# Kernel tuning notes

Hardware: AMD Instinct MI355X
Metric: run time of the kernel (lower is better)

The kernel has to match this reference:

```python
import jax, jax.numpy as jnp
import numpy as np

D_MODEL = 1024
NUM_HEADS = 16
D_K = D_MODEL // NUM_HEADS


def setup_inputs() -> dict:
    key = jax.random.key(0)
    ks = jax.random.split(key, 9)
    s = 1.0 / np.sqrt(D_MODEL)
    inp = {
        "x": jax.random.normal(ks[0], (4, 2048, D_MODEL), dtype=jnp.float32),
        "W_q": jax.random.uniform(ks[1], (D_MODEL, D_MODEL), jnp.float32, -s, s),
        "b_q": jax.random.uniform(ks[2], (D_MODEL,), jnp.float32, -s, s),
        "W_k": jax.random.uniform(ks[3], (D_MODEL, D_MODEL), jnp.float32, -s, s),
        "b_k": jax.random.uniform(ks[4], (D_MODEL,), jnp.float32, -s, s),
        "W_v": jax.random.uniform(ks[5], (D_MODEL, D_MODEL), jnp.float32, -s, s),
        "b_v": jax.random.uniform(ks[6], (D_MODEL,), jnp.float32, -s, s),
        "W_o": jax.random.uniform(ks[7], (D_MODEL, D_MODEL), jnp.float32, -s, s),
        "b_o": jax.random.uniform(ks[8], (D_MODEL,), jnp.float32, -s, s),
    }
    return inp


def reference(x, W_q, b_q, W_k, b_k, W_v, b_v, W_o, b_o):
    B, S, _ = x.shape
    # Linear layers (torch convention: y = x @ W.T + b), split into heads -> [B, H, S, d_k]
    def proj(W, b):
        y = jnp.einsum("bsd,ed->bse", x, W) + b
        return y.reshape(B, S, NUM_HEADS, D_K).transpose(0, 2, 1, 3)

    Q = proj(W_q, b_q)
    K = proj(W_k, b_k)
    V = proj(W_v, b_v)

    scale = 1.0 / jnp.sqrt(jnp.asarray(D_K, dtype=x.dtype))
    scores = jnp.einsum("bhqd,bhkd->bhqk", Q, K) * scale  # [B, H, S, S]
    attn = jax.nn.softmax(scores, axis=-1)
    out = jnp.einsum("bhqk,bhkd->bhqd", attn, V)  # [B, H, S, d_k]
    out = out.transpose(0, 2, 1, 3).reshape(B, S, D_MODEL)
    return jnp.einsum("bsd,ed->bse", out, W_o) + b_o
```

## Files before the change

### kernel.cpp

```cpp
#include <hip/hip_runtime.h>
#include <hip/hip_bf16.h>
#include <math.h>


constexpr int D = 1024;
constexpr int H = 16;
constexpr int DK = 64;
constexpr int PSTR = 72;

typedef unsigned short u16;
typedef __attribute__((ext_vector_type(8))) short v8s;
typedef __attribute__((ext_vector_type(4))) float v4f;
typedef const __attribute__((address_space(1))) void gvoid;
typedef __attribute__((address_space(3))) void lvoid;
typedef __attribute__((address_space(3))) u16 ls_u16;
typedef __attribute__((address_space(3))) v8s lv8s;

__device__ __forceinline__ u16 rne_bf16(float f) {
  unsigned u = __float_as_uint(f);
  u += 0x7FFFu + ((u >> 16) & 1u);
  return (u16)(u >> 16);
}

__device__ __forceinline__ unsigned pk_bf16(float a, float b) {
  __hip_bfloat162 t = __float22bfloat162_rn(float2{a, b});
  return *reinterpret_cast<unsigned*>(&t);
}

__device__ __forceinline__ void cfence() { asm volatile("" ::: "memory"); }

__device__ __forceinline__ void split_body(const float* __restrict__ in,
                                           u16* __restrict__ hi, u16* __restrict__ lo,
                                           int i)
{
  const float4 v = ((const float4*)in)[i];
  const float f[4] = {v.x, v.y, v.z, v.w};
  ushort4 h, l;
  u16 hh[4], ll[4];
#pragma unroll
  for (int j = 0; j < 4; ++j) {
    const unsigned u = __float_as_uint(f[j]);
    hh[j] = (u16)(u >> 16);
    const float hf = __uint_as_float(u & 0xFFFF0000u);
    ll[j] = rne_bf16(f[j] - hf);
  }
  h.x = hh[0]; h.y = hh[1]; h.z = hh[2]; h.w = hh[3];
  l.x = ll[0]; l.y = ll[1]; l.z = ll[2]; l.w = ll[3];
  ((ushort4*)hi)[i] = h;
  ((ushort4*)lo)[i] = l;
}

__global__ __launch_bounds__(256) void split_all_kernel(
    const float* __restrict__ x,
    const float* __restrict__ w0, const float* __restrict__ w1,
    const float* __restrict__ w2, const float* __restrict__ w3,
    u16* __restrict__ xs_hi, u16* __restrict__ xs_lo,
    u16* __restrict__ qkv_hi, u16* __restrict__ qkv_lo,
    u16* __restrict__ o_hi, u16* __restrict__ o_lo, int n4x)
{
  constexpr int N4W = (int)(D * (size_t)D / 4);
  const int i = blockIdx.x * 256 + threadIdx.x;
  if (i < n4x) {
    split_body(x, xs_hi, xs_lo, i);
    return;
  }
  const int t = i - n4x;
  const int y = t / N4W;
  const int j = t - y * N4W;
  if (y >= 4) return;
  const float* src = (y == 0) ? w0 : (y == 1) ? w1 : (y == 2) ? w2 : w3;
  const size_t off = (size_t)y * (size_t)(D * (size_t)D);
  u16* hi = (y < 3) ? qkv_hi + off : o_hi;
  u16* lo = (y < 3) ? qkv_lo + off : o_lo;
  split_body(src, hi, lo, j);
}

template<int R>
__device__ __forceinline__ void stage_arr(const u16* __restrict__ src, ls_u16* dst,
                                          int tid, int row0, int k0)
{
  const int cg = (tid & 3) ^ ((tid >> 3) & 3);
#pragma unroll
  for (int j = 0; j < R / 128; ++j) {
    const int row = j * 128 + (tid >> 2);
    __builtin_amdgcn_global_load_lds(
        (gvoid*)(src + (size_t)(row0 + row) * D + k0 + cg * 8),
        (lvoid*)(dst + j * 4096 + tid * 8), 16, 0, 0);
  }
}

template<int BM, int BN, int EPI>
__global__ __launch_bounds__(512, 2) void gemm_pipe_kernel(
    const u16* __restrict__ Ahi, const u16* __restrict__ Alo,
    const u16* __restrict__ Whi, const u16* __restrict__ Wlo,
    const float* __restrict__ b0v, const float* __restrict__ b1v, const float* __restrict__ b2v,
    u16* __restrict__ Qb, u16* __restrict__ Kb, u16* __restrict__ Vtb,
    float* __restrict__ C, int S_)
{
  constexpr int TA = BM * 32;
  constexpr int TB = BN * 32;
  constexpr int BUFSZ = 2 * TA + 2 * TB;
  __shared__ u16 lds[3][BUFSZ];

  const int tid = threadIdx.x;
  const int lane = tid & 63, w = tid >> 6;
  const int wm = (w >> 1) * 64, wn = (w & 1) * 64;
  const int fr = lane & 15, fq = lane >> 4;
  const int csw = (fq ^ ((fr >> 1) & 3)) * 8;

  const int gx = gridDim.x;
  const int gyd = gridDim.y;
  const int nwg = gx * gyd;
  int id = blockIdx.y * gx + blockIdx.x;
  id = (id & 7) * (nwg >> 3) + (id >> 3);
  constexpr int GM = 4;
  const int per_grp = GM * gyd;
  const int grp = id / per_grp;
  const int ing = id - grp * per_grp;
  const int m0 = (grp * GM + (ing & (GM - 1))) * BM;
  const int n0 = (ing / GM) * BN;

  v4f acc[4][4];
#pragma unroll
  for (int mi = 0; mi < 4; ++mi)
#pragma unroll
    for (int ni = 0; ni < 4; ++ni) acc[mi][ni] = (v4f){0.f, 0.f, 0.f, 0.f};

  ls_u16* pb0 = (ls_u16*)&lds[0][0];
  ls_u16* pb1 = (ls_u16*)&lds[1][0];
  ls_u16* pb2 = (ls_u16*)&lds[2][0];

  int aoff[4], boff[4];
#pragma unroll
  for (int i = 0; i < 4; ++i) {
    aoff[i] = (wm + i * 16 + fr) * 32 + csw;
    boff[i] = 2 * TA + (wn + i * 16 + fr) * 32 + csw;
  }

#pragma unroll
  for (int p = 0; p < 2; ++p) {
    ls_u16* pb = (p == 0) ? pb0 : pb1;
    stage_arr<BM>(Ahi, pb, tid, m0, p * 32);
    stage_arr<BM>(Alo, pb + TA, tid, m0, p * 32);
    stage_arr<BN>(Whi, pb + 2 * TA, tid, n0, p * 32);
    stage_arr<BN>(Wlo, pb + 2 * TA + TB, tid, n0, p * 32);
  }

#pragma unroll 2
  for (int k = 0; k < 32; ++k) {
    const int ks = (k + 2 < 32) ? (k + 2) * 32 : 31 * 32;

    asm volatile("s_waitcnt vmcnt(6)" ::: "memory");
    __builtin_amdgcn_s_barrier();
    cfence();

    v8s ah[4], bh[4], tf[4];
#pragma unroll
    for (int i = 0; i < 4; ++i) ah[i] = *(const lv8s*)(pb0 + aoff[i]);
#pragma unroll
    for (int i = 0; i < 4; ++i) bh[i] = *(const lv8s*)(pb0 + boff[i]);
    stage_arr<BM>(Ahi, pb2, tid, m0, ks);
    __builtin_amdgcn_s_setprio(1);
#pragma unroll
    for (int mi = 0; mi < 4; ++mi)
#pragma unroll
      for (int ni = 0; ni < 4; ++ni)
        acc[mi][ni] = __builtin_amdgcn_mfma_f32_16x16x32_bf16(ah[mi], bh[ni], acc[mi][ni], 0, 0, 0);
    __builtin_amdgcn_s_setprio(0);
    cfence();
    __builtin_amdgcn_s_barrier();
    cfence();

#pragma unroll
    for (int i = 0; i < 4; ++i) tf[i] = *(const lv8s*)(pb0 + TA + aoff[i]);
    stage_arr<BM>(Alo, pb2 + TA, tid, m0, ks);
    __builtin_amdgcn_s_setprio(1);
#pragma unroll
    for (int mi = 0; mi < 4; ++mi)
#pragma unroll
      for (int ni = 0; ni < 4; ++ni)
        acc[mi][ni] = __builtin_amdgcn_mfma_f32_16x16x32_bf16(tf[mi], bh[ni], acc[mi][ni], 0, 0, 0);
    __builtin_amdgcn_s_setprio(0);
    cfence();
    __builtin_amdgcn_s_barrier();
    cfence();

#pragma unroll
    for (int i = 0; i < 4; ++i) tf[i] = *(const lv8s*)(pb0 + boff[i] + TB);
    stage_arr<BN>(Whi, pb2 + 2 * TA, tid, n0, ks);
    stage_arr<BN>(Wlo, pb2 + 2 * TA + TB, tid, n0, ks);
    __builtin_amdgcn_s_setprio(1);
#pragma unroll
    for (int mi = 0; mi < 4; ++mi)
#pragma unroll
      for (int ni = 0; ni < 4; ++ni)
        acc[mi][ni] = __builtin_amdgcn_mfma_f32_16x16x32_bf16(ah[mi], tf[ni], acc[mi][ni], 0, 0, 0);
    __builtin_amdgcn_s_setprio(0);
    cfence();

    ls_u16* t = pb0; pb0 = pb1; pb1 = pb2; pb2 = t;
  }

  const int lane4 = fq * 4;
  if constexpr (EPI == 0) {
    const int wsel = n0 >> 10;
    const float* bias = (wsel == 0) ? b0v : (wsel == 1) ? b1v : b2v;
    u16* Cb = (wsel == 0) ? Qb : (wsel == 1) ? Kb : Vtb;
    const int bb = m0 / S_;
    const int s0 = m0 - bb * S_;
#pragma unroll
    for (int mi = 0; mi < 4; ++mi) {
#pragma unroll
      for (int ni = 0; ni < 4; ++ni) {
        const int n = n0 + wn + ni * 16 + fr;
        const int nl = n & (D - 1);
        const float bvv = bias[nl];
        const int h = nl >> 6, dk = nl & 63;
#pragma unroll
        for (int r = 0; r < 4; ++r) {
          const int s = s0 + wm + mi * 16 + lane4 + r;
          const float val = acc[mi][ni][r] + bvv;
          if (wsel < 2)
            Cb[((size_t)(bb * H + h) * S_ + s) * DK + dk] = rne_bf16(val);
          else
            Cb[((size_t)(bb * H + h) * DK + dk) * S_ + s] = rne_bf16(val);
        }
      }
    }
  } else {
#pragma unroll
    for (int mi = 0; mi < 4; ++mi)
#pragma unroll
      for (int ni = 0; ni < 4; ++ni) {
        const int n = n0 + wn + ni * 16 + fr;
        const float bvv = b0v[n];
#pragma unroll
        for (int r = 0; r < 4; ++r) {
          const int m = m0 + wm + mi * 16 + lane4 + r;
          C[(size_t)m * D + n] = acc[mi][ni][r] + bvv;
        }
      }
  }
}

__global__ __launch_bounds__(512, 4) void attn_mfma_kernel(
    const u16* __restrict__ Qb, const u16* __restrict__ Kb, const u16* __restrict__ Vtb,
    u16* __restrict__ Ohi, u16* __restrict__ Olo, int S_)
{
  __shared__ u16 Ks[2][64 * 64];
  __shared__ u16 Vt[2][64 * 64];
  __shared__ u16 Pl[8][32 * PSTR];

  const int tid = threadIdx.x;
  const int lane = tid & 63, w = tid >> 6;
  const int fr = lane & 15, fq = lane >> 4;

  const int gqx = gridDim.x;
  const int nwg = gqx * gridDim.y * gridDim.z;
  int id = (blockIdx.z * gridDim.y + blockIdx.y) * gqx + blockIdx.x;
  id = (id & 7) * (nwg >> 3) + (id >> 3);
  const int qx = id % gqx;
  const int rest = id / gqx;
  const int h = rest % H;
  const int b = rest / H;

  const int q0 = qx * 256;
  const int wq = w * 32;
  const size_t base = (size_t)(b * H + h) * S_ * DK;

  const int srow = tid >> 3;
  const int scb = (tid & 7) ^ (srow & 7);

  auto stage_kv = [&](int j0, int bufi) {
    __builtin_amdgcn_global_load_lds((gvoid*)(Kb + base + (size_t)(j0 + srow) * DK + scb * 8),
                                     (lvoid*)(&Ks[bufi][0] + tid * 8), 16, 0, 0);
    __builtin_amdgcn_global_load_lds((gvoid*)(Vtb + base + (size_t)srow * S_ + j0 + scb * 8),
                                     (lvoid*)(&Vt[bufi][0] + tid * 8), 16, 0, 0);
  };

  stage_kv(0, 0);

  v8s qa[2][2];
#pragma unroll
  for (int ni = 0; ni < 2; ++ni)
#pragma unroll
    for (int ks = 0; ks < 2; ++ks)
      qa[ni][ks] = *(const v8s*)(Qb + base + (size_t)(q0 + wq + ni * 16 + fr) * DK + ks * 32 + fq * 8);

  v4f o[4][2];
  float lsum[2] = {0.f, 0.f};
#pragma unroll
  for (int mi = 0; mi < 4; ++mi)
#pragma unroll
    for (int ni = 0; ni < 2; ++ni) o[mi][ni] = (v4f){0.f, 0.f, 0.f, 0.f};

  asm volatile("s_waitcnt vmcnt(0)" ::: "memory");
  __builtin_amdgcn_s_barrier();
  cfence();

  const int NT = S_ >> 6;
  for (int jt = 0; jt < NT; ++jt) {
    const int cur = jt & 1;
    if (jt + 1 < NT) stage_kv((jt + 1) * 64, cur ^ 1);

    const u16* Kc = &Ks[cur][0];
    const u16* Vc = &Vt[cur][0];

    v4f s[4][2];
#pragma unroll
    for (int mi = 0; mi < 4; ++mi)
#pragma unroll
      for (int ni = 0; ni < 2; ++ni) s[mi][ni] = (v4f){0.f, 0.f, 0.f, 0.f};
#pragma unroll
    for (int ks = 0; ks < 2; ++ks) {
      v8s kb[4];
#pragma unroll
      for (int mi = 0; mi < 4; ++mi) {
        const int row = mi * 16 + fr;
        kb[mi] = *(const v8s*)&Kc[row * 64 + (((ks * 4 + fq) ^ (row & 7)) * 8)];
      }
#pragma unroll
      for (int mi = 0; mi < 4; ++mi)
#pragma unroll
        for (int ni = 0; ni < 2; ++ni)
          s[mi][ni] = __builtin_amdgcn_mfma_f32_16x16x32_bf16(kb[mi], qa[ni][ks], s[mi][ni], 0, 0, 0);
    }

#pragma unroll
    for (int mi = 0; mi < 4; ++mi)
#pragma unroll
      for (int ni = 0; ni < 2; ++ni) {
        float p[4];
#pragma unroll
        for (int r = 0; r < 4; ++r) p[r] = __expf(s[mi][ni][r] * 0.125f);
        lsum[ni] += (p[0] + p[1]) + (p[2] + p[3]);
        uint2 pk;
        pk.x = pk_bf16(p[0], p[1]);
        pk.y = pk_bf16(p[2], p[3]);
        *(uint2*)&Pl[w][(ni * 16 + fr) * PSTR + mi * 16 + fq * 4] = pk;
      }

#pragma unroll
    for (int ks = 0; ks < 2; ++ks) {
      v8s vb[4], pa[2];
#pragma unroll
      for (int mi = 0; mi < 4; ++mi) {
        const int row = mi * 16 + fr;
        vb[mi] = *(const v8s*)&Vc[row * 64 + (((ks * 4 + fq) ^ (row & 7)) * 8)];
      }
#pragma unroll
      for (int ni = 0; ni < 2; ++ni)
        pa[ni] = *(const v8s*)&Pl[w][(ni * 16 + fr) * PSTR + ks * 32 + fq * 8];
#pragma unroll
      for (int mi = 0; mi < 4; ++mi)
#pragma unroll
        for (int ni = 0; ni < 2; ++ni)
          o[mi][ni] = __builtin_amdgcn_mfma_f32_16x16x32_bf16(vb[mi], pa[ni], o[mi][ni], 0, 0, 0);
    }

    asm volatile("s_waitcnt vmcnt(0)" ::: "memory");
    cfence();
    __builtin_amdgcn_s_barrier();
    cfence();
  }

  float linv[2];
#pragma unroll
  for (int ni = 0; ni < 2; ++ni) {
    float l = lsum[ni];
    l += __shfl_xor(l, 16);
    l += __shfl_xor(l, 32);
    linv[ni] = 1.f / l;
  }

#pragma unroll
  for (int ni = 0; ni < 2; ++ni) {
    const int q = q0 + wq + ni * 16 + fr;
    const size_t rowbase = (size_t)(b * S_ + q) * D + h * DK;
#pragma unroll
    for (int mi = 0; mi < 4; ++mi) {
      const int d0 = mi * 16 + fq * 4;
      float v[4];
      unsigned u[4];
      float res[4];
#pragma unroll
      for (int r = 0; r < 4; ++r) {
        v[r] = o[mi][ni][r] * linv[ni];
        u[r] = __float_as_uint(v[r]);
        res[r] = v[r] - __uint_as_float(u[r] & 0xFFFF0000u);
      }
      uint2 hi, lo;
      hi.x = (u[1] & 0xFFFF0000u) | (u[0] >> 16);
      hi.y = (u[3] & 0xFFFF0000u) | (u[2] >> 16);
      lo.x = pk_bf16(res[0], res[1]);
      lo.y = pk_bf16(res[2], res[3]);
      *(uint2*)(Ohi + rowbase + d0) = hi;
      *(uint2*)(Olo + rowbase + d0) = lo;
    }
  }
}

extern "C" void kernel_launch(void* const* d_in, const int* in_sizes, int n_in,
                              void* d_out, int out_size, void* d_ws, size_t ws_size,
                              hipStream_t stream) {
  const float* x  = (const float*)d_in[0];
  const float* Wq = (const float*)d_in[1];
  const float* bq = (const float*)d_in[2];
  const float* Wk = (const float*)d_in[3];
  const float* bk = (const float*)d_in[4];
  const float* Wv = (const float*)d_in[5];
  const float* bv = (const float*)d_in[6];
  const float* Wo = (const float*)d_in[7];
  const float* bo = (const float*)d_in[8];

  const int M = in_sizes[0] / D;
  const int B = 4;
  const int S_ = M / B;
  const size_t MD = (size_t)M * D;
  const size_t DD = (size_t)D * D;

  u16* Qb    = (u16*)d_ws;
  u16* Kb    = Qb + MD;
  u16* Vtb   = Kb + MD;
  u16* xs_hi = Vtb + MD;
  u16* xs_lo = xs_hi + MD;
  u16* Ohi   = xs_lo + MD;
  u16* Olo   = Ohi + MD;
  u16* wo_hi = Olo + MD;
  u16* wo_lo = wo_hi + DD;

  u16* wqkv_hi = (u16*)d_out;
  u16* wqkv_lo = wqkv_hi + 3 * DD;

  const int n4x = (int)(MD / 4);
  const int n4w = (int)(DD / 4);
  const int nsb = (n4x + 4 * n4w + 255) / 256;
  split_all_kernel<<<nsb, 256, 0, stream>>>(x, Wq, Wk, Wv, Wo,
                                            xs_hi, xs_lo, wqkv_hi, wqkv_lo,
                                            wo_hi, wo_lo, n4x);

  dim3 gq(M / 256, 3 * D / 128);
  gemm_pipe_kernel<256, 128, 0><<<gq, 512, 0, stream>>>(
      xs_hi, xs_lo, wqkv_hi, wqkv_lo, bq, bk, bv, Qb, Kb, Vtb, nullptr, S_);

  dim3 ga(S_ / 256, H, B);
  attn_mfma_kernel<<<ga, 512, 0, stream>>>(Qb, Kb, Vtb, Ohi, Olo, S_);

  dim3 go(M / 256, D / 128);
  gemm_pipe_kernel<256, 128, 1><<<go, 512, 0, stream>>>(
      Ohi, Olo, wo_hi, wo_lo, bo, nullptr, nullptr, nullptr, nullptr, nullptr,
      (float*)d_out, S_);
}
```

Measured before the change: 394.1 us.

## Enlarge GEMM tiles to 256x256 and switch to double-buffered LDS pipeline

The projection GEMMs now use 256x256 output tiles with each wave computing 128x64, doubling per-wave accumulators to raise arithmetic intensity and cut global re-reads of the split bf16 operands. The LDS pipeline drops from triple to double buffering, prefetching only one k-step ahead and synchronising with a full vmcnt(0) wait plus barrier each iteration. This halves the grid size (fewer workgroups, e.g. 128 for the output projection) and raises register and LDS pressure (128KB LDS), so occupancy and latency hiding may suffer.

```diff
diff --git a/kernel.cpp b/kernel.cpp
--- a/kernel.cpp
+++ b/kernel.cpp
@@ -89,7 +89,7 @@
   }
 }
 
-template<int BM, int BN, int EPI>
+template<int EPI>
 __global__ __launch_bounds__(512, 2) void gemm_pipe_kernel(
     const u16* __restrict__ Ahi, const u16* __restrict__ Alo,
     const u16* __restrict__ Whi, const u16* __restrict__ Wlo,
@@ -97,14 +97,15 @@
     u16* __restrict__ Qb, u16* __restrict__ Kb, u16* __restrict__ Vtb,
     float* __restrict__ C, int S_)
 {
+  constexpr int BM = 256, BN = 256;
   constexpr int TA = BM * 32;
   constexpr int TB = BN * 32;
   constexpr int BUFSZ = 2 * TA + 2 * TB;
-  __shared__ u16 lds[3][BUFSZ];
+  __shared__ u16 lds[2][BUFSZ];
 
   const int tid = threadIdx.x;
   const int lane = tid & 63, w = tid >> 6;
-  const int wm = (w >> 1) * 64, wn = (w & 1) * 64;
+  const int wm = (w >> 2) * 128, wn = (w & 3) * 64;
   const int fr = lane & 15, fq = lane >> 4;
   const int csw = (fq ^ ((fr >> 1) & 3)) * 8;
 
@@ -120,49 +121,43 @@
   const int m0 = (grp * GM + (ing & (GM - 1))) * BM;
   const int n0 = (ing / GM) * BN;
 
-  v4f acc[4][4];
-#pragma unroll
-  for (int mi = 0; mi < 4; ++mi)
+  v4f acc[8][4];
+#pragma unroll
+  for (int mi = 0; mi < 8; ++mi)
 #pragma unroll
     for (int ni = 0; ni < 4; ++ni) acc[mi][ni] = (v4f){0.f, 0.f, 0.f, 0.f};
 
   ls_u16* pb0 = (ls_u16*)&lds[0][0];
   ls_u16* pb1 = (ls_u16*)&lds[1][0];
-  ls_u16* pb2 = (ls_u16*)&lds[2][0];
-
-  int aoff[4], boff[4];
-#pragma unroll
-  for (int i = 0; i < 4; ++i) {
-    aoff[i] = (wm + i * 16 + fr) * 32 + csw;
-    boff[i] = 2 * TA + (wn + i * 16 + fr) * 32 + csw;
-  }
-
-#pragma unroll
-  for (int p = 0; p < 2; ++p) {
-    ls_u16* pb = (p == 0) ? pb0 : pb1;
-    stage_arr<BM>(Ahi, pb, tid, m0, p * 32);
-    stage_arr<BM>(Alo, pb + TA, tid, m0, p * 32);
-    stage_arr<BN>(Whi, pb + 2 * TA, tid, n0, p * 32);
-    stage_arr<BN>(Wlo, pb + 2 * TA + TB, tid, n0, p * 32);
-  }
+
+  int aoff[8], boff[4];
+#pragma unroll
+  for (int i = 0; i < 8; ++i) aoff[i] = (wm + i * 16 + fr) * 32 + csw;
+#pragma unroll
+  for (int i = 0; i < 4; ++i) boff[i] = 2 * TA + (wn + i * 16 + fr) * 32 + csw;
+
+  stage_arr<BM>(Ahi, pb0, tid, m0, 0);
+  stage_arr<BM>(Alo, pb0 + TA, tid, m0, 0);
+  stage_arr<BN>(Whi, pb0 + 2 * TA, tid, n0, 0);
+  stage_arr<BN>(Wlo, pb0 + 2 * TA + TB, tid, n0, 0);
+  asm volatile("s_waitcnt vmcnt(0)" ::: "memory");
+  __builtin_amdgcn_s_barrier();
+  cfence();
 
 #pragma unroll 2
   for (int k = 0; k < 32; ++k) {
-    const int ks = (k + 2 < 32) ? (k + 2) * 32 : 31 * 32;
-
-    asm volatile("s_waitcnt vmcnt(6)" ::: "memory");
-    __builtin_amdgcn_s_barrier();
-    cfence();
-
-    v8s ah[4], bh[4], tf[4];
-#pragma unroll
-    for (int i = 0; i < 4; ++i) ah[i] = *(const lv8s*)(pb0 + aoff[i]);
+    const int ks = (k + 1 < 32) ? (k + 1) * 32 : 31 * 32;
+
+    v8s ah[8], bh[4], tf[8];
+#pragma unroll
+    for (int i = 0; i < 8; ++i) ah[i] = *(const lv8s*)(pb0 + aoff[i]);
 #pragma unroll
     for (int i = 0; i < 4; ++i) bh[i] = *(const lv8s*)(pb0 + boff[i]);
-    stage_arr<BM>(Ahi, pb2, tid, m0, ks);
+    stage_arr<BM>(Ahi, pb1, tid, m0, ks);
+    stage_arr<BM>(Alo, pb1 + TA, tid, m0, ks);
     __builtin_amdgcn_s_setprio(1);
 #pragma unroll
-    for (int mi = 0; mi < 4; ++mi)
+    for (int mi = 0; mi < 8; ++mi)
 #pragma unroll
       for (int ni = 0; ni < 4; ++ni)
         acc[mi][ni] = __builtin_amdgcn_mfma_f32_16x16x32_bf16(ah[mi], bh[ni], acc[mi][ni], 0, 0, 0);
@@ -172,11 +167,12 @@
     cfence();
 
 #pragma unroll
-    for (int i = 0; i < 4; ++i) tf[i] = *(const lv8s*)(pb0 + TA + aoff[i]);
-    stage_arr<BM>(Alo, pb2 + TA, tid, m0, ks);
+    for (int i = 0; i < 8; ++i) tf[i] = *(const lv8s*)(pb0 + TA + aoff[i]);
+    stage_arr<BN>(Whi, pb1 + 2 * TA, tid, n0, ks);
+    stage_arr<BN>(Wlo, pb1 + 2 * TA + TB, tid, n0, ks);
     __builtin_amdgcn_s_setprio(1);
 #pragma unroll
-    for (int mi = 0; mi < 4; ++mi)
+    for (int mi = 0; mi < 8; ++mi)
 #pragma unroll
       for (int ni = 0; ni < 4; ++ni)
         acc[mi][ni] = __builtin_amdgcn_mfma_f32_16x16x32_bf16(tf[mi], bh[ni], acc[mi][ni], 0, 0, 0);
@@ -187,18 +183,20 @@
 
 #pragma unroll
     for (int i = 0; i < 4; ++i) tf[i] = *(const lv8s*)(pb0 + boff[i] + TB);
-    stage_arr<BN>(Whi, pb2 + 2 * TA, tid, n0, ks);
-    stage_arr<BN>(Wlo, pb2 + 2 * TA + TB, tid, n0, ks);
     __builtin_amdgcn_s_setprio(1);
 #pragma unroll
-    for (int mi = 0; mi < 4; ++mi)
+    for (int mi = 0; mi < 8; ++mi)
 #pragma unroll
       for (int ni = 0; ni < 4; ++ni)
         acc[mi][ni] = __builtin_amdgcn_mfma_f32_16x16x32_bf16(ah[mi], tf[ni], acc[mi][ni], 0, 0, 0);
     __builtin_amdgcn_s_setprio(0);
     cfence();
 
-    ls_u16* t = pb0; pb0 = pb1; pb1 = pb2; pb2 = t;
+    asm volatile("s_waitcnt vmcnt(0)" ::: "memory");
+    __builtin_amdgcn_s_barrier();
+    cfence();
+
+    ls_u16* t = pb0; pb0 = pb1; pb1 = t;
   }
 
   const int lane4 = fq * 4;
@@ -209,7 +207,7 @@
     const int bb = m0 / S_;
     const int s0 = m0 - bb * S_;
 #pragma unroll
-    for (int mi = 0; mi < 4; ++mi) {
+    for (int mi = 0; mi < 8; ++mi) {
 #pragma unroll
       for (int ni = 0; ni < 4; ++ni) {
         const int n = n0 + wn + ni * 16 + fr;
@@ -229,7 +227,7 @@
     }
   } else {
 #pragma unroll
-    for (int mi = 0; mi < 4; ++mi)
+    for (int mi = 0; mi < 8; ++mi)
 #pragma unroll
       for (int ni = 0; ni < 4; ++ni) {
         const int n = n0 + wn + ni * 16 + fr;
@@ -439,15 +437,15 @@
                                             xs_hi, xs_lo, wqkv_hi, wqkv_lo,
                                             wo_hi, wo_lo, n4x);
 
-  dim3 gq(M / 256, 3 * D / 128);
-  gemm_pipe_kernel<256, 128, 0><<<gq, 512, 0, stream>>>(
+  dim3 gq(M / 256, 3 * D / 256);
+  gemm_pipe_kernel<0><<<gq, 512, 0, stream>>>(
       xs_hi, xs_lo, wqkv_hi, wqkv_lo, bq, bk, bv, Qb, Kb, Vtb, nullptr, S_);
 
   dim3 ga(S_ / 256, H, B);
   attn_mfma_kernel<<<ga, 512, 0, stream>>>(Qb, Kb, Vtb, Ohi, Olo, S_);
 
-  dim3 go(M / 256, D / 128);
-  gemm_pipe_kernel<256, 128, 1><<<go, 512, 0, stream>>>(
+  dim3 go(M / 256, D / 256);
+  gemm_pipe_kernel<1><<<go, 512, 0, stream>>>(
       Ohi, Olo, wo_hi, wo_lo, bo, nullptr, nullptr, nullptr, nullptr, nullptr,
       (float*)d_out, S_);
 }
```

Measured after the change: 427.0 us. +8.4%, slower.
